# Kernel optimization log

Measured on AMD Instinct MI355X. Metric: run time of the kernel, lower is better.

The kernel has to match this reference:

```python
import jax, jax.numpy as jnp
import numpy as np


def _aggregate(xyz, node, features, k):
    # xyz: [B,3,N], node: [B,3,M], features: [B,C,N] -> [B,C,M]
    # squared euclidean distances via expansion (same math as (x-n)^2 sum)
    d = (jnp.sum(xyz ** 2, axis=1)[:, :, None]
         + jnp.sum(node ** 2, axis=1)[:, None, :]
         - 2.0 * jnp.einsum('bdn,bdm->bnm', xyz, node))  # [B,N,M]
    # k smallest over N for each of M nodes (order irrelevant: max-pool after)
    _, nn_idx = jax.lax.top_k(-jnp.transpose(d, (0, 2, 1)), k)  # [B,M,k]
    # gather C-channel features at neighbor indices -> [B,C,M,k]
    g = jnp.take_along_axis(features[:, :, None, :], nn_idx[:, None, :, :], axis=3)
    return jnp.max(g, axis=3)  # [B,C,M]


def setup_inputs() -> dict:
    key = jax.random.key(0)
    k1, k2, k3, k4 = jax.random.split(key, 4)
    B, N, C = 4, 16384, 128
    return {
        'input_coords': jax.random.normal(k1, (B, 3, N), dtype=jnp.float32),
        'input_feats': jax.random.normal(k2, (B, C, N), dtype=jnp.float32),
        'W': jax.random.normal(k3, (C, C), dtype=jnp.float32) * 0.05,
        'b': jax.random.normal(k4, (C,), dtype=jnp.float32) * 0.05,
        'num_sample': 2048,
        'num_agg': 16,
    }


def reference(input_coords, input_feats, W, b, num_sample, num_agg):
    # Dropout in eval mode -> identity. proj = 1x1 Conv1d == per-point linear.
    Z = input_feats  # [B,C,N]
    proj = jax.nn.relu(jnp.einsum('oc,bcn->bon', W, Z) + b[None, :, None])
    vector = jnp.max(proj, axis=-1, keepdims=True)  # [B,C,1]
    weights = jnp.sum(input_feats * vector, axis=1)  # [B,N]
    scores = jax.nn.sigmoid(weights)
    values, idx = jax.lax.top_k(scores, num_sample)  # [B,M] each, sorted desc
    pool_coords_static = jnp.take_along_axis(input_coords, idx[:, None, :], axis=2)  # [B,3,M]
    pool_feats_static = jnp.take_along_axis(input_feats, idx[:, None, :], axis=2)    # [B,C,M]
    v = values[:, None, :]  # [B,1,M]
    pool_feats = pool_feats_static * v
    pool_coords = pool_coords_static * v
    agg_feats = _aggregate(input_coords, pool_coords_static, input_feats, num_agg)  # [B,C,M]
    pool_feats = jnp.concatenate([pool_feats, agg_feats], axis=1)  # [B,2C,M]
    return (pool_coords_static, pool_coords, pool_feats)
```

## Files before the change

### kernel.cpp

```cpp
#include <hip/hip_runtime.h>
#include <hip/hip_bf16.h>
#include <stdint.h>

#define BB 4
#define NN 16384
#define CC 128
#define MM 2048
#define KNN 16
#define QCAP 512
#define EPS 1e-3f

typedef unsigned int u32;
typedef unsigned short u16;
typedef unsigned long long u64;

#define OFF_FEATT   0ull
#define OFF_PTS4    33554432ull
#define OFF_WT      37748736ull
#define OFF_KEYS    37814272ull
#define OFF_VEC     38338560ull
#define OFF_IDX     38340608ull
#define OFF_VAL     38373376ull
#define OFF_TMP1    38406144ull
#define OFF_TMP2    38668288ull

__device__ __forceinline__ float np_dist(float4 p, float4 nd) {
#pragma clang fp contract(off)
    float dot = ((p.x * nd.x) + (p.y * nd.y)) + (p.z * nd.z);
    float d = (p.w + nd.w) - 2.0f * dot;
    return d;
}

__device__ __forceinline__ float sfast(float4 p, float4 nd) {
    float dot = fmaf(p.x, nd.x, fmaf(p.y, nd.y, p.z * nd.z));
    return fmaf(-2.0f, dot, p.w);
}

__device__ __forceinline__ u32 mono_bits(float d) {
    u32 u = __float_as_uint(d);
    u ^= ((u32)(((int)u) >> 31)) | 0x80000000u;
    return u;
}

__device__ __forceinline__ float kth16(float v, int l) {
    float sv = v;
#pragma unroll
    for (int k = 2; k <= 64; k <<= 1) {
#pragma unroll
        for (int j = k >> 1; j > 0; j >>= 1) {
            float pv = __shfl_xor(sv, j);
            bool up = ((l & k) == 0);
            bool tmin = (((l & j) == 0) == up);
            float mn = fminf(sv, pv), mx = fmaxf(sv, pv);
            sv = tmin ? mn : mx;
        }
    }
    return __shfl(sv, 15);
}

__global__ void k_prep(const float* __restrict__ coords, const float* __restrict__ W,
                       float4* __restrict__ pts4, float* __restrict__ WT,
                       u32* __restrict__ vecU) {
    int g = blockIdx.x * 256 + threadIdx.x;
    if (g < BB * NN) {
        int b = g >> 14, n = g & (NN - 1);
        const float* cb = coords + (size_t)b * 3 * NN;
        float x = cb[n], y = cb[NN + n], z = cb[2 * NN + n];
        float w;
        {
#pragma clang fp contract(off)
            w = ((x * x) + (y * y)) + (z * z);
        }
        pts4[g] = make_float4(x, y, z, w);
    } else if (g < BB * NN + CC * CC) {
        int i = g - BB * NN;
        int o = i >> 7, c = i & 127;
        WT[c * CC + o] = W[i];
    } else if (g < BB * NN + CC * CC + BB * CC) {
        vecU[g - BB * NN - CC * CC] = 0u;
    }
}

__global__ void k_transpose(const float* __restrict__ feats, float* __restrict__ feat_t) {
    __shared__ float t[64][65];
    int bx = blockIdx.x;
    int b = bx >> 9; int rem = bx & 511; int nb = rem >> 1; int cb2 = rem & 1;
    int n0 = nb * 64, c0 = cb2 * 64;
    int l = threadIdx.x & 63, r0 = threadIdx.x >> 6;
    const float* fb = feats + (size_t)b * CC * NN;
#pragma unroll
    for (int p = 0; p < 16; ++p) {
        int r = r0 + p * 4;
        t[r][l] = fb[(size_t)(c0 + r) * NN + n0 + l];
    }
    __syncthreads();
    float* ob = feat_t + (size_t)b * NN * CC;
#pragma unroll
    for (int p = 0; p < 16; ++p) {
        int r = r0 + p * 4;
        ob[(size_t)(n0 + r) * CC + c0 + l] = t[l][r];
    }
}

__global__ __launch_bounds__(256, 4) void k_vec(const float* __restrict__ feats,
        const float* __restrict__ WT, const float* __restrict__ bias, u32* __restrict__ vecU) {
    __shared__ float Wl[CC * 64];
    int bx = blockIdx.x;
    int oh = bx & 1;
    int ntile = (bx >> 1) & 63;
    int b = bx >> 7;
    int n0 = ntile * 256;
    int tid = threadIdx.x, l = tid & 63;
    int w = __builtin_amdgcn_readfirstlane(tid >> 6);
    for (int i = tid; i < CC * 64; i += 256) {
        int c = i >> 6, op = i & 63;
        Wl[i] = WT[c * CC + oh * 64 + op];
    }
    __syncthreads();
    int o0 = w * 16;
    const float* zb = feats + (size_t)b * CC * NN + n0 + 4 * l;
    float bo[16];
#pragma unroll
    for (int oi = 0; oi < 16; ++oi) bo[oi] = bias[oh * 64 + o0 + oi];
    float acc0[16], acc1[16], acc2[16], acc3[16];
#pragma unroll
    for (int oi = 0; oi < 16; ++oi) { acc0[oi] = bo[oi]; acc1[oi] = bo[oi]; acc2[oi] = bo[oi]; acc3[oi] = bo[oi]; }
    float4 zpre = *(const float4*)zb;
#pragma unroll 2
    for (int c = 0; c < CC; ++c) {
        float4 z = zpre;
        if (c + 1 < CC) zpre = *(const float4*)(zb + (size_t)(c + 1) * NN);
        const float* wr = Wl + c * 64 + o0;
        float4 w0 = *(const float4*)(wr);
        float4 w1 = *(const float4*)(wr + 4);
        float4 w2 = *(const float4*)(wr + 8);
        float4 w3 = *(const float4*)(wr + 12);
        float wv[16] = {w0.x, w0.y, w0.z, w0.w, w1.x, w1.y, w1.z, w1.w,
                        w2.x, w2.y, w2.z, w2.w, w3.x, w3.y, w3.z, w3.w};
#pragma unroll
        for (int oi = 0; oi < 16; ++oi) {
            acc0[oi] = fmaf(wv[oi], z.x, acc0[oi]);
            acc1[oi] = fmaf(wv[oi], z.y, acc1[oi]);
            acc2[oi] = fmaf(wv[oi], z.z, acc2[oi]);
            acc3[oi] = fmaf(wv[oi], z.w, acc3[oi]);
        }
    }
#pragma unroll
    for (int oi = 0; oi < 16; ++oi) {
        float r0 = acc0[oi] > 0.0f ? acc0[oi] : 0.0f;
        float r1 = acc1[oi] > 0.0f ? acc1[oi] : 0.0f;
        float r2 = acc2[oi] > 0.0f ? acc2[oi] : 0.0f;
        float r3 = acc3[oi] > 0.0f ? acc3[oi] : 0.0f;
        float rv = fmaxf(fmaxf(r0, r1), fmaxf(r2, r3));
#pragma unroll
        for (int s = 32; s; s >>= 1) rv = fmaxf(rv, __shfl_xor(rv, s));
        if (l == 0) atomicMax(vecU + b * CC + oh * 64 + o0 + oi, __float_as_uint(rv));
    }
}

__global__ void k_scores(const float* __restrict__ feats, const float* __restrict__ vecF,
                         u64* __restrict__ keys) {
    int i = blockIdx.x * 256 + threadIdx.x;
    int b = i >> 14, n = i & (NN - 1);
    const float* fb = feats + (size_t)b * CC * NN + n;
    const float* vb = vecF + b * CC;
    float wsum = 0.f;
#pragma unroll 8
    for (int c = 0; c < CC; ++c) wsum = fmaf(fb[(size_t)c * NN], vb[c], wsum);
    float s = 1.0f / (1.0f + expf(-wsum));
    u32 mono = __float_as_uint(s);
    keys[i] = ((u64)mono << 32) | (u64)(0xFFFFFFFFu - (u32)n);
}

__global__ __launch_bounds__(1024) void k_sortchunk(u64* __restrict__ keys) {
    __shared__ u64 sk[2048];
    int b = blockIdx.x >> 3, c = blockIdx.x & 7;
    int tid = threadIdx.x;
    u64* src = keys + (size_t)b * NN + c * 2048;
    sk[tid] = src[tid];
    sk[tid + 1024] = src[tid + 1024];
    for (int size = 2; size <= 2048; size <<= 1) {
        for (int stride = size >> 1; stride > 0; stride >>= 1) {
            __syncthreads();
            int t = tid;
            int i = (t << 1) - (t & (stride - 1));
            int j = i + stride;
            u64 a = sk[i], cc = sk[j];
            bool up = ((i & size) == 0);
            if ((a < cc) == up) { sk[i] = cc; sk[j] = a; }
        }
    }
    __syncthreads();
    src[tid] = sk[tid];
    src[tid + 1024] = sk[tid + 1024];
}

__global__ __launch_bounds__(512) void k_mergetop(const u64* __restrict__ in,
        u64* __restrict__ outp, int lg ) {
    __shared__ u64 mk[4096];
    int b = blockIdx.x >> lg, pr = blockIdx.x & ((1 << lg) - 1);
    int tid = threadIdx.x;
    const u64* s0 = in + ((size_t)((b << lg) + pr) * 2) * 2048;
    const u64* s1 = s0 + 2048;
    for (int t = tid; t < 2048; t += 512) { mk[t] = s0[t]; mk[2048 + t] = s1[2047 - t]; }
    __syncthreads();
    for (int t = tid; t < 2048; t += 512) {
        u64 a = mk[t], c = mk[t + 2048];
        if (a < c) { mk[t] = c; mk[t + 2048] = a; }
    }
    for (int stride = 1024; stride > 0; stride >>= 1) {
        __syncthreads();
        for (int t = tid; t < 1024; t += 512) {
            int i = (t << 1) - (t & (stride - 1));
            int j = i + stride;
            u64 a = mk[i], c = mk[j];
            if (a < c) { mk[i] = c; mk[j] = a; }
        }
    }
    __syncthreads();
    u64* dst = outp + (size_t)((b << lg) + pr) * 2048;
    for (int t = tid; t < 2048; t += 512) dst[t] = mk[t];
}

__global__ __launch_bounds__(512) void k_mergefinal(const u64* __restrict__ in,
        u32* __restrict__ idxA, float* __restrict__ valA) {
    __shared__ u64 mk[4096];
    int b = blockIdx.x, tid = threadIdx.x;
    const u64* s0 = in + (size_t)(b * 2) * 2048;
    const u64* s1 = s0 + 2048;
    for (int t = tid; t < 2048; t += 512) { mk[t] = s0[t]; mk[2048 + t] = s1[2047 - t]; }
    __syncthreads();
    for (int t = tid; t < 2048; t += 512) {
        u64 a = mk[t], c = mk[t + 2048];
        if (a < c) { mk[t] = c; mk[t + 2048] = a; }
    }
    for (int stride = 1024; stride > 0; stride >>= 1) {
        __syncthreads();
        for (int t = tid; t < 1024; t += 512) {
            int i = (t << 1) - (t & (stride - 1));
            int j = i + stride;
            u64 a = mk[i], c = mk[j];
            if (a < c) { mk[i] = c; mk[j] = a; }
        }
    }
    __syncthreads();
    for (int t = tid; t < 2048; t += 512) {
        u64 k = mk[t];
        idxA[b * MM + t] = 0xFFFFFFFFu - (u32)(k & 0xFFFFFFFFull);
        valA[b * MM + t] = __uint_as_float((u32)(k >> 32));
    }
}

__global__ void k_gather(const float4* __restrict__ pts4, const float* __restrict__ feat_t,
        const u32* __restrict__ idxA, const float* __restrict__ valA, float* __restrict__ out) {
    int g = blockIdx.x * 256 + threadIdx.x;
    int b = g >> 11, i = g & (MM - 1);
    u32 n = idxA[g];
    float v = valA[g];
    float4 p = pts4[(b << 14) + (int)n];
    float* o0 = out + (size_t)b * 3 * MM + i;
    o0[0] = p.x; o0[MM] = p.y; o0[2 * MM] = p.z;
    float* o1 = o0 + 24576;
    o1[0] = p.x * v; o1[MM] = p.y * v; o1[2 * MM] = p.z * v;
    const float4* ft = (const float4*)(feat_t + ((size_t)(b << 14) + n) * CC);
    float* o2 = out + 49152 + ((size_t)b * 256) * MM + i;
#pragma unroll 8
    for (int q = 0; q < 32; ++q) {
        float4 f = ft[q];
        o2[(size_t)(4 * q + 0) * MM] = f.x * v;
        o2[(size_t)(4 * q + 1) * MM] = f.y * v;
        o2[(size_t)(4 * q + 2) * MM] = f.z * v;
        o2[(size_t)(4 * q + 3) * MM] = f.w * v;
    }
}

__global__ __launch_bounds__(256, 7) void k_knn(const float4* __restrict__ pts4,
        const float* __restrict__ feat_t, const u32* __restrict__ idxA, float* __restrict__ out) {
    __shared__ float4 ptsS[1024];
    __shared__ u16 qS[4][QCAP];
    __shared__ float4 nodeS[4];
    int bx = blockIdx.x;
    int b = bx >> 9, mblk = bx & 511;
    int tid = threadIdx.x, l = tid & 63;
    const float4* pb = pts4 + (b << 14);
    if (tid < 4) nodeS[tid] = pb[idxA[b * MM + mblk * 4 + tid]];
#pragma unroll
    for (int j = 0; j < 4; ++j) ptsS[tid + 256 * j] = pb[tid + 256 * j];
    __syncthreads();
    int w = __builtin_amdgcn_readfirstlane(tid >> 6);
    float4 nd = nodeS[w];
    float lm = 3.0e38f;
#pragma unroll 4
    for (int j = 0; j < 16; ++j) lm = fminf(lm, sfast(ptsS[l + 64 * j], nd));
    __syncthreads();
#pragma unroll
    for (int j = 0; j < 4; ++j) ptsS[tid + 256 * j] = pb[1024 + tid + 256 * j];
    __syncthreads();
#pragma unroll 4
    for (int j = 0; j < 16; ++j) lm = fminf(lm, sfast(ptsS[l + 64 * j], nd));
    float T = kth16(lm, l) + 2.0f * EPS;
    int qc = 0;
    for (int ch = 0; ch < 16; ++ch) {
        __syncthreads();
#pragma unroll
        for (int j = 0; j < 4; ++j) ptsS[tid + 256 * j] = pb[ch * 1024 + tid + 256 * j];
        __syncthreads();
        for (int j = 0; j < 16; ++j) {
            float4 p = ptsS[l + 64 * j];
            float dt = fmaf(p.x, nd.x, fmaf(p.y, nd.y, p.z * nd.z));
            float s = fmaf(-2.0f, dt, p.w);
            bool pred = (s <= T);
            u64 bal = __ballot(pred);
            if (bal) {
                if (pred) {
                    int off = __builtin_amdgcn_mbcnt_hi((u32)(bal >> 32),
                              __builtin_amdgcn_mbcnt_lo((u32)bal, 0));
                    int slot = qc + off;
                    if (slot < QCAP) qS[w][slot] = (u16)(ch * 1024 + l + 64 * j);
                }
                qc += (int)__popcll(bal);
            }
        }
    }
    int cnt = qc < QCAP ? qc : QCAP;
    u64 regk[QCAP / 64];
#pragma unroll
    for (int s = 0; s < QCAP / 64; ++s) {
        u64 kk = ~0ull;
        if ((s << 6) < cnt) {
            int pos = (s << 6) + l;
            if (pos < cnt) {
                u32 n = qS[w][pos];
                float d = np_dist(pb[n], nd);
                kk = ((u64)mono_bits(d) << 32) | (u64)n;
            }
        }
        regk[s] = kk;
    }
    float mx0 = -3.0e38f, mx1 = -3.0e38f;
    for (int it = 0; it < KNN; ++it) {
        u64 mykey = ~0ull;
#pragma unroll
        for (int s = 0; s < QCAP / 64; ++s)
            if ((s << 6) < cnt) mykey = regk[s] < mykey ? regk[s] : mykey;
        u64 r = mykey;
#pragma unroll
        for (int j = 32; j > 0; j >>= 1) {
            u64 o = __shfl_xor(r, j);
            r = o < r ? o : r;
        }
#pragma unroll
        for (int s = 0; s < QCAP / 64; ++s)
            if ((s << 6) < cnt) { if (regk[s] == r) regk[s] = ~0ull; }
        if (r != ~0ull) {
            u32 nj = (u32)(r & 0xFFFFFFFFull);
            const float2 f = *(const float2*)(feat_t + ((size_t)(b << 14) + nj) * CC + (l << 1));
            mx0 = fmaxf(mx0, f.x);
            mx1 = fmaxf(mx1, f.y);
        }
    }
    int m = mblk * 4 + w;
    size_t ob = 49152 + ((size_t)(b * 256 + 128 + 2 * l)) * MM + m;
    out[ob] = mx0;
    out[ob + MM] = mx1;
}

extern "C" void kernel_launch(void* const* d_in, const int* in_sizes, int n_in,
                              void* d_out, int out_size, void* d_ws, size_t ws_size,
                              hipStream_t stream) {
    const float* coords = (const float*)d_in[0];
    const float* feats  = (const float*)d_in[1];
    const float* W      = (const float*)d_in[2];
    const float* bias   = (const float*)d_in[3];
    char* ws = (char*)d_ws;
    float*  feat_t = (float*)(ws + OFF_FEATT);
    float4* pts4   = (float4*)(ws + OFF_PTS4);
    float*  WT     = (float*)(ws + OFF_WT);
    u64*    keys   = (u64*)(ws + OFF_KEYS);
    u32*    vecU   = (u32*)(ws + OFF_VEC);
    u32*    idxA   = (u32*)(ws + OFF_IDX);
    float*  valA   = (float*)(ws + OFF_VAL);
    u64*    tmp1   = (u64*)(ws + OFF_TMP1);
    u64*    tmp2   = (u64*)(ws + OFF_TMP2);
    float*  out    = (float*)d_out;

    int prepN = BB * NN + CC * CC + BB * CC;
    k_prep     <<<(prepN + 255) / 256, 256, 0, stream>>>(coords, W, pts4, WT, vecU);
    k_vec      <<<512, 256, 0, stream>>>(feats, WT, bias, vecU);
    k_transpose<<<BB * (NN / 64) * (CC / 64), 256, 0, stream>>>(feats, feat_t);
    k_scores   <<<BB * NN / 256, 256, 0, stream>>>(feats, (const float*)vecU, keys);
    k_sortchunk<<<BB * 8, 1024, 0, stream>>>(keys);
    k_mergetop <<<BB * 4, 512, 0, stream>>>(keys, tmp1, 2);
    k_mergetop <<<BB * 2, 512, 0, stream>>>(tmp1, tmp2, 1);
    k_mergefinal<<<BB, 512, 0, stream>>>(tmp2, idxA, valA);
    k_gather   <<<BB * MM / 256, 256, 0, stream>>>(pts4, feat_t, idxA, valA, out);
    k_knn      <<<BB * (MM / 4), 256, 0, stream>>>(pts4, feat_t, idxA, out);
}
```

Before: 239.0 us.

## Split kNN into scan and select kernels with global candidate queues

Splits the kNN kernel in two. The first kernel has each wave handle two query nodes at once, so every shared-memory point load is reused for both, and splits the N scan into two halves across blocks. Candidates go to global per-node queues through atomic counters. A second kernel reads each queue and does the top-16 selection and the feature max-gather. This cuts LDS point reloads per node and adds parallelism, at the cost of global atomics, an extra launch and global queue traffic. The candidate threshold is still computed over the first 2048 points by each half, so correctness is kept.

```diff
diff --git a/kernel.cpp b/kernel.cpp
--- a/kernel.cpp
+++ b/kernel.cpp
@@ -7,7 +7,7 @@
 #define CC 128
 #define MM 2048
 #define KNN 16
-#define QCAP 512
+#define QCAPG 512
 #define EPS 1e-3f
 
 typedef unsigned int u32;
@@ -23,6 +23,8 @@
 #define OFF_VAL     38373376ull
 #define OFF_TMP1    38406144ull
 #define OFF_TMP2    38668288ull
+#define OFF_QCNT    38799360ull
+#define OFF_Q       38832128ull
 
 __device__ __forceinline__ float np_dist(float4 p, float4 nd) {
 #pragma clang fp contract(off)
@@ -60,7 +62,7 @@
 
 __global__ void k_prep(const float* __restrict__ coords, const float* __restrict__ W,
                        float4* __restrict__ pts4, float* __restrict__ WT,
-                       u32* __restrict__ vecU) {
+                       u32* __restrict__ vecU, u32* __restrict__ qcnt) {
     int g = blockIdx.x * 256 + threadIdx.x;
     if (g < BB * NN) {
         int b = g >> 14, n = g & (NN - 1);
@@ -78,6 +80,8 @@
         WT[c * CC + o] = W[i];
     } else if (g < BB * NN + CC * CC + BB * CC) {
         vecU[g - BB * NN - CC * CC] = 0u;
+    } else if (g < BB * NN + CC * CC + BB * CC + BB * MM) {
+        qcnt[g - BB * NN - CC * CC - BB * CC] = 0u;
     }
 }
 
@@ -274,63 +278,99 @@
     }
 }
 
-__global__ __launch_bounds__(256, 7) void k_knn(const float4* __restrict__ pts4,
-        const float* __restrict__ feat_t, const u32* __restrict__ idxA, float* __restrict__ out) {
+__device__ __forceinline__ void emit_q(u32* __restrict__ qcnt, u32* __restrict__ q,
+        int gn, u64 bal, bool pred, int n, int l) {
+    int cnt = (int)__popcll(bal);
+    u32 base = 0;
+    if (l == 0) base = atomicAdd(qcnt + gn, (u32)cnt);
+    base = (u32)__shfl((int)base, 0);
+    if (pred) {
+        int off = (int)__popcll(bal & ((1ull << l) - 1ull));
+        u32 slot = base + (u32)off;
+        if (slot < QCAPG) q[(size_t)gn * QCAPG + slot] = (u32)n;
+    }
+}
+
+__global__ __launch_bounds__(256) void k_knnS(const float4* __restrict__ pts4,
+        const u32* __restrict__ idxA, u32* __restrict__ qcnt, u32* __restrict__ q) {
     __shared__ float4 ptsS[1024];
-    __shared__ u16 qS[4][QCAP];
-    __shared__ float4 nodeS[4];
+    __shared__ float4 nodeS[8];
     int bx = blockIdx.x;
-    int b = bx >> 9, mblk = bx & 511;
+    int b = bx >> 9;
+    int idx = bx & 511;
+    int ng = idx >> 1;
+    int half = idx & 1;
     int tid = threadIdx.x, l = tid & 63;
+    int w = __builtin_amdgcn_readfirstlane(tid >> 6);
     const float4* pb = pts4 + (b << 14);
-    if (tid < 4) nodeS[tid] = pb[idxA[b * MM + mblk * 4 + tid]];
+    if (tid < 8) nodeS[tid] = pb[idxA[b * MM + ng * 8 + tid]];
 #pragma unroll
     for (int j = 0; j < 4; ++j) ptsS[tid + 256 * j] = pb[tid + 256 * j];
     __syncthreads();
-    int w = __builtin_amdgcn_readfirstlane(tid >> 6);
-    float4 nd = nodeS[w];
-    float lm = 3.0e38f;
+    float4 nd0 = nodeS[w * 2 + 0];
+    float4 nd1 = nodeS[w * 2 + 1];
+    float lm0 = 3.0e38f, lm1 = 3.0e38f;
 #pragma unroll 4
-    for (int j = 0; j < 16; ++j) lm = fminf(lm, sfast(ptsS[l + 64 * j], nd));
+    for (int j = 0; j < 16; ++j) {
+        float4 p = ptsS[l + 64 * j];
+        lm0 = fminf(lm0, sfast(p, nd0));
+        lm1 = fminf(lm1, sfast(p, nd1));
+    }
     __syncthreads();
 #pragma unroll
     for (int j = 0; j < 4; ++j) ptsS[tid + 256 * j] = pb[1024 + tid + 256 * j];
     __syncthreads();
 #pragma unroll 4
-    for (int j = 0; j < 16; ++j) lm = fminf(lm, sfast(ptsS[l + 64 * j], nd));
-    float T = kth16(lm, l) + 2.0f * EPS;
-    int qc = 0;
-    for (int ch = 0; ch < 16; ++ch) {
+    for (int j = 0; j < 16; ++j) {
+        float4 p = ptsS[l + 64 * j];
+        lm0 = fminf(lm0, sfast(p, nd0));
+        lm1 = fminf(lm1, sfast(p, nd1));
+    }
+    float T0 = kth16(lm0, l) + 2.0f * EPS;
+    float T1 = kth16(lm1, l) + 2.0f * EPS;
+    int gn0 = (b << 11) + ng * 8 + w * 2;
+    for (int ch = half * 8; ch < half * 8 + 8; ++ch) {
         __syncthreads();
 #pragma unroll
         for (int j = 0; j < 4; ++j) ptsS[tid + 256 * j] = pb[ch * 1024 + tid + 256 * j];
         __syncthreads();
         for (int j = 0; j < 16; ++j) {
             float4 p = ptsS[l + 64 * j];
-            float dt = fmaf(p.x, nd.x, fmaf(p.y, nd.y, p.z * nd.z));
-            float s = fmaf(-2.0f, dt, p.w);
-            bool pred = (s <= T);
-            u64 bal = __ballot(pred);
-            if (bal) {
-                if (pred) {
-                    int off = __builtin_amdgcn_mbcnt_hi((u32)(bal >> 32),
-                              __builtin_amdgcn_mbcnt_lo((u32)bal, 0));
-                    int slot = qc + off;
-                    if (slot < QCAP) qS[w][slot] = (u16)(ch * 1024 + l + 64 * j);
-                }
-                qc += (int)__popcll(bal);
-            }
-        }
-    }
-    int cnt = qc < QCAP ? qc : QCAP;
-    u64 regk[QCAP / 64];
-#pragma unroll
-    for (int s = 0; s < QCAP / 64; ++s) {
+            int n = ch * 1024 + l + 64 * j;
+            float dt0 = fmaf(p.x, nd0.x, fmaf(p.y, nd0.y, p.z * nd0.z));
+            float s0 = fmaf(-2.0f, dt0, p.w);
+            float dt1 = fmaf(p.x, nd1.x, fmaf(p.y, nd1.y, p.z * nd1.z));
+            float s1 = fmaf(-2.0f, dt1, p.w);
+            bool p0 = (s0 <= T0);
+            bool p1 = (s1 <= T1);
+            u64 bal0 = __ballot(p0);
+            if (bal0) emit_q(qcnt, q, gn0, bal0, p0, n, l);
+            u64 bal1 = __ballot(p1);
+            if (bal1) emit_q(qcnt, q, gn0 + 1, bal1, p1, n, l);
+        }
+    }
+}
+
+__global__ __launch_bounds__(256) void k_knnM(const float4* __restrict__ pts4,
+        const float* __restrict__ feat_t, const u32* __restrict__ idxA,
+        const u32* __restrict__ qcnt, const u32* __restrict__ q, float* __restrict__ out) {
+    int w = __builtin_amdgcn_readfirstlane(threadIdx.x >> 6);
+    int g = blockIdx.x * 4 + w;
+    int b = g >> 11, m = g & (MM - 1);
+    int l = threadIdx.x & 63;
+    const float4* pb = pts4 + (b << 14);
+    float4 nd = pb[idxA[g]];
+    int cnt = (int)qcnt[g];
+    if (cnt > QCAPG) cnt = QCAPG;
+    const u32* qq = q + (size_t)g * QCAPG;
+    u64 regk[QCAPG / 64];
+#pragma unroll
+    for (int s = 0; s < QCAPG / 64; ++s) {
         u64 kk = ~0ull;
         if ((s << 6) < cnt) {
             int pos = (s << 6) + l;
             if (pos < cnt) {
-                u32 n = qS[w][pos];
+                u32 n = qq[pos];
                 float d = np_dist(pb[n], nd);
                 kk = ((u64)mono_bits(d) << 32) | (u64)n;
             }
@@ -341,7 +381,7 @@
     for (int it = 0; it < KNN; ++it) {
         u64 mykey = ~0ull;
 #pragma unroll
-        for (int s = 0; s < QCAP / 64; ++s)
+        for (int s = 0; s < QCAPG / 64; ++s)
             if ((s << 6) < cnt) mykey = regk[s] < mykey ? regk[s] : mykey;
         u64 r = mykey;
 #pragma unroll
@@ -350,7 +390,7 @@
             r = o < r ? o : r;
         }
 #pragma unroll
-        for (int s = 0; s < QCAP / 64; ++s)
+        for (int s = 0; s < QCAPG / 64; ++s)
             if ((s << 6) < cnt) { if (regk[s] == r) regk[s] = ~0ull; }
         if (r != ~0ull) {
             u32 nj = (u32)(r & 0xFFFFFFFFull);
@@ -359,7 +399,6 @@
             mx1 = fmaxf(mx1, f.y);
         }
     }
-    int m = mblk * 4 + w;
     size_t ob = 49152 + ((size_t)(b * 256 + 128 + 2 * l)) * MM + m;
     out[ob] = mx0;
     out[ob + MM] = mx1;
@@ -382,10 +421,12 @@
     float*  valA   = (float*)(ws + OFF_VAL);
     u64*    tmp1   = (u64*)(ws + OFF_TMP1);
     u64*    tmp2   = (u64*)(ws + OFF_TMP2);
+    u32*    qcnt   = (u32*)(ws + OFF_QCNT);
+    u32*    q      = (u32*)(ws + OFF_Q);
     float*  out    = (float*)d_out;
 
-    int prepN = BB * NN + CC * CC + BB * CC;
-    k_prep     <<<(prepN + 255) / 256, 256, 0, stream>>>(coords, W, pts4, WT, vecU);
+    int prepN = BB * NN + CC * CC + BB * CC + BB * MM;
+    k_prep     <<<(prepN + 255) / 256, 256, 0, stream>>>(coords, W, pts4, WT, vecU, qcnt);
     k_vec      <<<512, 256, 0, stream>>>(feats, WT, bias, vecU);
     k_transpose<<<BB * (NN / 64) * (CC / 64), 256, 0, stream>>>(feats, feat_t);
     k_scores   <<<BB * NN / 256, 256, 0, stream>>>(feats, (const float*)vecU, keys);
@@ -394,5 +435,6 @@
     k_mergetop <<<BB * 2, 512, 0, stream>>>(tmp1, tmp2, 1);
     k_mergefinal<<<BB, 512, 0, stream>>>(tmp2, idxA, valA);
     k_gather   <<<BB * MM / 256, 256, 0, stream>>>(pts4, feat_t, idxA, valA, out);
-    k_knn      <<<BB * (MM / 4), 256, 0, stream>>>(pts4, feat_t, idxA, out);
-}
+    k_knnS     <<<2048, 256, 0, stream>>>(pts4, idxA, qcnt, q);
+    k_knnM     <<<BB * MM / 4, 256, 0, stream>>>(pts4, feat_t, idxA, qcnt, q, out);
+}
```

New measurement: 277.0 us. +15.9%, slower.

## Double-buffer kNN point tiles and process eight nodes per block

Applied to the files above, without the earlier changes.

The kNN kernel now uses 512-thread blocks that handle eight query nodes each instead of four. This halves how often each block streams the point cloud through shared memory. Point chunks are prefetched into registers and staged into two alternating shared buffers, so each chunk needs one barrier instead of two and global loads overlap the distance scan. Candidate compaction switches from ballot/mbcnt prefix counting to per-lane shared-memory atomicAdd on a per-wave counter, which makes candidate order nondeterministic and may add atomic contention. The larger blocks use more shared memory, which may lower occupancy.

```diff
diff --git a/kernel.cpp b/kernel.cpp
--- a/kernel.cpp
+++ b/kernel.cpp
@@ -274,55 +274,56 @@
     }
 }
 
-__global__ __launch_bounds__(256, 7) void k_knn(const float4* __restrict__ pts4,
+__global__ __launch_bounds__(512, 6) void k_knn(const float4* __restrict__ pts4,
         const float* __restrict__ feat_t, const u32* __restrict__ idxA, float* __restrict__ out) {
-    __shared__ float4 ptsS[1024];
-    __shared__ u16 qS[4][QCAP];
-    __shared__ float4 nodeS[4];
+    __shared__ float4 ptsS[2][1024];
+    __shared__ u16 qS[8][QCAP];
+    __shared__ u32 qcS[8];
+    __shared__ float4 nodeS[8];
     int bx = blockIdx.x;
-    int b = bx >> 9, mblk = bx & 511;
+    int b = bx >> 8, mblk = bx & 255;
     int tid = threadIdx.x, l = tid & 63;
+    int w = __builtin_amdgcn_readfirstlane(tid >> 6);
     const float4* pb = pts4 + (b << 14);
-    if (tid < 4) nodeS[tid] = pb[idxA[b * MM + mblk * 4 + tid]];
-#pragma unroll
-    for (int j = 0; j < 4; ++j) ptsS[tid + 256 * j] = pb[tid + 256 * j];
-    __syncthreads();
-    int w = __builtin_amdgcn_readfirstlane(tid >> 6);
+    if (tid < 8) { nodeS[tid] = pb[idxA[b * MM + mblk * 8 + tid]]; qcS[tid] = 0u; }
+    float4 pre0 = pb[tid], pre1 = pb[tid + 512];
+    ptsS[0][tid] = pre0; ptsS[0][tid + 512] = pre1;
+    pre0 = pb[1024 + tid]; pre1 = pb[1024 + tid + 512];
+    __syncthreads();
     float4 nd = nodeS[w];
     float lm = 3.0e38f;
 #pragma unroll 4
-    for (int j = 0; j < 16; ++j) lm = fminf(lm, sfast(ptsS[l + 64 * j], nd));
-    __syncthreads();
-#pragma unroll
-    for (int j = 0; j < 4; ++j) ptsS[tid + 256 * j] = pb[1024 + tid + 256 * j];
+    for (int j = 0; j < 16; ++j) lm = fminf(lm, sfast(ptsS[0][l + 64 * j], nd));
+    ptsS[1][tid] = pre0; ptsS[1][tid + 512] = pre1;
+    pre0 = pb[2048 + tid]; pre1 = pb[2048 + tid + 512];
     __syncthreads();
 #pragma unroll 4
-    for (int j = 0; j < 16; ++j) lm = fminf(lm, sfast(ptsS[l + 64 * j], nd));
+    for (int j = 0; j < 16; ++j) lm = fminf(lm, sfast(ptsS[1][l + 64 * j], nd));
     float T = kth16(lm, l) + 2.0f * EPS;
-    int qc = 0;
     for (int ch = 0; ch < 16; ++ch) {
-        __syncthreads();
-#pragma unroll
-        for (int j = 0; j < 4; ++j) ptsS[tid + 256 * j] = pb[ch * 1024 + tid + 256 * j];
-        __syncthreads();
+        int buf = ch & 1;
+#pragma unroll 4
         for (int j = 0; j < 16; ++j) {
-            float4 p = ptsS[l + 64 * j];
+            float4 p = ptsS[buf][l + 64 * j];
+            int n = ch * 1024 + l + 64 * j;
             float dt = fmaf(p.x, nd.x, fmaf(p.y, nd.y, p.z * nd.z));
             float s = fmaf(-2.0f, dt, p.w);
-            bool pred = (s <= T);
-            u64 bal = __ballot(pred);
-            if (bal) {
-                if (pred) {
-                    int off = __builtin_amdgcn_mbcnt_hi((u32)(bal >> 32),
-                              __builtin_amdgcn_mbcnt_lo((u32)bal, 0));
-                    int slot = qc + off;
-                    if (slot < QCAP) qS[w][slot] = (u16)(ch * 1024 + l + 64 * j);
-                }
-                qc += (int)__popcll(bal);
+            if (s <= T) {
+                u32 slot = atomicAdd(&qcS[w], 1u);
+                if (slot < QCAP) qS[w][slot] = (u16)n;
             }
         }
-    }
-    int cnt = qc < QCAP ? qc : QCAP;
+        if (ch + 2 < 16) {
+            __syncthreads();
+            ptsS[buf][tid] = pre0; ptsS[buf][tid + 512] = pre1;
+            if (ch + 3 < 16) {
+                pre0 = pb[(ch + 3) * 1024 + tid];
+                pre1 = pb[(ch + 3) * 1024 + tid + 512];
+            }
+        }
+    }
+    int cnt = (int)qcS[w];
+    if (cnt > QCAP) cnt = QCAP;
     u64 regk[QCAP / 64];
 #pragma unroll
     for (int s = 0; s < QCAP / 64; ++s) {
@@ -359,7 +360,7 @@
             mx1 = fmaxf(mx1, f.y);
         }
     }
-    int m = mblk * 4 + w;
+    int m = mblk * 8 + w;
     size_t ob = 49152 + ((size_t)(b * 256 + 128 + 2 * l)) * MM + m;
     out[ob] = mx0;
     out[ob + MM] = mx1;
@@ -394,5 +395,5 @@
     k_mergetop <<<BB * 2, 512, 0, stream>>>(tmp1, tmp2, 1);
     k_mergefinal<<<BB, 512, 0, stream>>>(tmp2, idxA, valA);
     k_gather   <<<BB * MM / 256, 256, 0, stream>>>(pts4, feat_t, idxA, valA, out);
-    k_knn      <<<BB * (MM / 4), 256, 0, stream>>>(pts4, feat_t, idxA, out);
-}
+    k_knn      <<<BB * (MM / 8), 512, 0, stream>>>(pts4, feat_t, idxA, out);
+}
```

Result: slower. 247.3 us (+3.5%).
